# Performance work log

Measured on AMD Instinct MI355X. Metric: run time of the kernel, lower is better.

The kernel has to match this reference:

```python
import jax, jax.numpy as jnp
import numpy as np

N, E = 10000, 100000
WIDTH, KER_WIDTH, DEPTH = 32, 128, 3
EDGE_ATTR_DIM, IN_WIDTH, OUT_WIDTH, COORD_DIM = 6, 3, 1, 3


def _glorot(k, fan_in, fan_out):
    return jax.random.normal(k, (fan_in, fan_out), jnp.float32) / np.sqrt(fan_in).astype(np.float32)


def setup_inputs() -> dict:
    key = jax.random.key(0)
    ks = jax.random.split(key, 16)
    z = lambda n: jnp.zeros((n,), jnp.float32)
    return {
        "x": jax.random.normal(ks[0], (N, IN_WIDTH), jnp.float32),
        "edge_index": jax.random.randint(ks[1], (2, E), 0, N),
        "edge_attr": jax.random.normal(ks[2], (E, EDGE_ATTR_DIM), jnp.float32),
        "coords_init": jax.random.normal(ks[3], (N, COORD_DIM), jnp.float32),
        "fc1_w": _glorot(ks[4], IN_WIDTH, WIDTH), "fc1_b": z(WIDTH),
        "ker_w1": _glorot(ks[5], EDGE_ATTR_DIM + 1, KER_WIDTH // 2), "ker_b1": z(KER_WIDTH // 2),
        "ker_w2": _glorot(ks[6], KER_WIDTH // 2, KER_WIDTH), "ker_b2": z(KER_WIDTH),
        "ker_w3": _glorot(ks[7], KER_WIDTH, WIDTH * WIDTH), "ker_b3": z(WIDTH * WIDTH),
        "cm_w1": _glorot(ks[8], WIDTH, WIDTH), "cm_b1": z(WIDTH),
        "cm_w2": _glorot(ks[9], WIDTH, 1) * 1e-3,  # xavier gain=0.001 coord head, no bias
        "fc2_w1": _glorot(ks[10], WIDTH, 2 * WIDTH), "fc2_b1": z(2 * WIDTH),
        "fc2_w2": _glorot(ks[11], 2 * WIDTH, OUT_WIDTH), "fc2_b2": z(OUT_WIDTH),
    }


def _seg_mean(data, seg, n):
    s = jax.ops.segment_sum(data, seg, num_segments=n)
    c = jax.ops.segment_sum(jnp.ones((seg.shape[0], 1), data.dtype), seg, num_segments=n)
    return s / jnp.clip(c, 1.0)


def reference(x, edge_index, edge_attr, coords_init,
              fc1_w, fc1_b, ker_w1, ker_b1, ker_w2, ker_b2, ker_w3, ker_b3,
              cm_w1, cm_b1, cm_w2, fc2_w1, fc2_b1, fc2_w2, fc2_b2):
    row, col = edge_index[0], edge_index[1]
    h = x @ fc1_w + fc1_b                                   # [N, W]
    coord = coords_init
    for _ in range(DEPTH):
        coord_diff = coord[row] - coord[col]                # [E, 3]
        radial = jnp.sum(coord_diff * coord_diff, axis=-1, keepdims=True)
        kin = jnp.concatenate([edge_attr, radial], axis=-1)  # [E, ker_in]
        k = jax.nn.relu(kin @ ker_w1 + ker_b1)
        k = jax.nn.relu(k @ ker_w2 + ker_b2)
        Wk = (k @ ker_w3 + ker_b3).reshape(E, WIDTH, WIDTH)  # per-edge kernel matrix
        m = jnp.einsum('eij,ej->ei', Wk, h[col])             # per-edge message [E, W]
        phi = jax.nn.relu(m @ cm_w1 + cm_b1) @ cm_w2         # [E, 1]
        coord = coord + _seg_mean(coord_diff * phi, row, N)  # equivariant coord update
        h = jax.nn.relu(h + _seg_mean(m, row, N))            # GKN node update
    out = jax.nn.relu(h @ fc2_w1 + fc2_b1) @ fc2_w2 + fc2_b2  # [N, out_width]
    return out, coord
```

## Files before the change

kernel.cpp:

```cpp
#include <hip/hip_runtime.h>
#include <hip/hip_bf16.h>

#define NN 10000
#define NE 100000
#define NSEG_MAX 16384

typedef __bf16 bf16x8 __attribute__((ext_vector_type(8)));
typedef float  f32x4  __attribute__((ext_vector_type(4)));

__device__ __forceinline__ f32x4 relu4(f32x4 a) {
    a.x = fmaxf(a.x, 0.f); a.y = fmaxf(a.y, 0.f);
    a.z = fmaxf(a.z, 0.f); a.w = fmaxf(a.w, 0.f);
    return a;
}

__device__ __forceinline__ unsigned pk2(float a, float b) {
    unsigned ua = (unsigned)__builtin_bit_cast(unsigned short, (__bf16)a);
    unsigned ub = (unsigned)__builtin_bit_cast(unsigned short, (__bf16)b);
    return ua | (ub << 16);
}

__global__ void k_setup(const float* __restrict__ w3, __bf16* __restrict__ w3t_sw,
                        const float* __restrict__ b3, __bf16* __restrict__ b3t_sw,
                        const float* __restrict__ w2, __bf16* __restrict__ w2t_sw,
                        const float* __restrict__ cw1, __bf16* __restrict__ cmw1_sw,
                        const float* __restrict__ x, const float* __restrict__ fc1w,
                        const float* __restrict__ fc1b, const float* __restrict__ cinit,
                        float* __restrict__ h, float* __restrict__ coord,
                        const int* __restrict__ eidx,
                        int* __restrict__ deg, int* __restrict__ within,
                        int* __restrict__ degc, int* __restrict__ withinc) {
    int t = blockIdx.x * blockDim.x + threadIdx.x;
    if (t < 131072) {
        int jj = t & 7, l = (t >> 3) & 63, ut = t >> 9;
        int u  = ut*16 + (l & 15);
        int j2 = ((l >> 4) & 3)*8 + jj;
        int f  = u >> 9, ll = (u >> 3) & 63, j0 = u & 7;
        int c  = (f & 3)*32 + ((ll >> 4) & 3)*8 + j0;
        int i  = (f >> 2)*16 + (ll & 15);
        w3t_sw[t] = (__bf16)w3[c*1024 + i*32 + j2];
    } else if (t < 132096) {
        int idx = t - 131072;
        int jj = idx & 7, l = (idx >> 3) & 63, tt = idx >> 9;
        int i  = tt*16 + (l & 15);
        int j2 = ((l >> 4) & 3)*8 + jj;
        b3t_sw[idx] = (__bf16)b3[i*32 + j2];
    } else if (t < 140288) {
        int idx = t - 132096;
        int jj = idx & 7, l = (idx >> 3) & 63, g = idx >> 9;
        int ct = g >> 1, ks = g & 1;
        int c  = ct*16 + (l & 15);
        int ch = ks*32 + ((l >> 4) & 3)*8 + jj;
        w2t_sw[idx] = (__bf16)w2[ch*128 + c];
    } else if (t < 142336) {
        int idx = t - 140288;
        int jj = idx & 7, l = (idx >> 3) & 63, ot = idx >> 9;
        int o  = ot*16 + (l & 15);
        int i  = ((l >> 4) & 3)*8 + jj;
        cmw1_sw[idx] = (__bf16)cw1[i*32 + o];
    } else if (t < 142336 + NN) {
        int n = t - 142336;
        float x0 = x[n*3+0], x1 = x[n*3+1], x2 = x[n*3+2];
        #pragma unroll
        for (int j = 0; j < 32; j += 4) {
            f32x4 a = *(const f32x4*)(fc1b + j);
            a += x0 * (*(const f32x4*)(fc1w + 0*32 + j));
            a += x1 * (*(const f32x4*)(fc1w + 1*32 + j));
            a += x2 * (*(const f32x4*)(fc1w + 2*32 + j));
            *(f32x4*)(h + n*32 + j) = a;
        }
        coord[n*3+0] = cinit[n*3+0];
        coord[n*3+1] = cinit[n*3+1];
        coord[n*3+2] = cinit[n*3+2];
    } else if (t < 142336 + NN + NE) {
        int e = t - 142336 - NN;
        within[e] = atomicAdd(&deg[eidx[e]], 1);
    } else if (t < 142336 + NN + 2*NE) {
        int e = t - 142336 - NN - NE;
        withinc[e] = atomicAdd(&degc[eidx[NE + e]], 1);
    }
}

__global__ __launch_bounds__(1024, 1)
void k_scan(const int* __restrict__ deg, int* __restrict__ rowptr,
            float* __restrict__ deg_inv,
            const int* __restrict__ degc, int* __restrict__ colptr,
            int* __restrict__ seg_meta, int* __restrict__ seg_start) {
    __shared__ int ssum[1024];
    const int tid = threadIdx.x;
    const int CH = 10;
    const int base = tid * CH;

    int s = 0;
    for (int i = 0; i < CH; ++i) { int n = base + i; if (n < NN) s += deg[n]; }
    ssum[tid] = s;
    __syncthreads();
    for (int off = 1; off < 1024; off <<= 1) {
        int t = (tid >= off) ? ssum[tid - off] : 0;
        __syncthreads(); ssum[tid] += t; __syncthreads();
    }
    int run = ssum[tid] - s;
    for (int i = 0; i < CH; ++i) {
        int n = base + i;
        if (n < NN) {
            int d = deg[n];
            rowptr[n] = run; run += d;
            deg_inv[n] = 1.0f / (float)(d > 1 ? d : 1);
        }
    }
    if (tid == 1023) rowptr[NN] = ssum[1023];
    __syncthreads();

    s = 0;
    for (int i = 0; i < CH; ++i) { int n = base + i; if (n < NN) s += degc[n]; }
    ssum[tid] = s;
    __syncthreads();
    for (int off = 1; off < 1024; off <<= 1) {
        int t = (tid >= off) ? ssum[tid - off] : 0;
        __syncthreads(); ssum[tid] += t; __syncthreads();
    }
    run = ssum[tid] - s;
    for (int i = 0; i < CH; ++i) {
        int n = base + i;
        if (n < NN) { colptr[n] = run; run += degc[n]; }
    }
    if (tid == 1023) colptr[NN] = ssum[1023];
    __syncthreads();

    s = 0;
    for (int i = 0; i < CH; ++i) { int n = base + i; if (n < NN) s += (degc[n] + 15) >> 4; }
    ssum[tid] = s;
    __syncthreads();
    for (int off = 1; off < 1024; off <<= 1) {
        int t = (tid >= off) ? ssum[tid - off] : 0;
        __syncthreads(); ssum[tid] += t; __syncthreads();
    }
    run = ssum[tid] - s;
    for (int i = 0; i < CH; ++i) {
        int n = base + i;
        if (n < NN) {
            int d = degc[n], ns = (d + 15) >> 4, cp = colptr[n];
            for (int k = 0; k < ns; ++k) {
                int cnt = d - k*16; if (cnt > 16) cnt = 16;
                seg_meta[run + k]  = n | (cnt << 16);
                seg_start[run + k] = cp + k*16;
            }
            run += ns;
        }
    }
    __syncthreads();
    int nseg = ssum[1023];
    for (int sg = nseg + tid; sg < NSEG_MAX; sg += 1024) {
        seg_meta[sg] = -1;
        seg_start[sg] = 0;
    }
}

__global__ void k_setup2(const int* __restrict__ eidx, const float* __restrict__ eattr,
                         const int* __restrict__ rowptr, const int* __restrict__ within,
                         const int* __restrict__ colptr, const int* __restrict__ withinc,
                         int* __restrict__ cs_pos, int* __restrict__ cs_row,
                         float* __restrict__ eattr_cs) {
    int e = blockIdx.x * blockDim.x + threadIdx.x;
    if (e >= NE) return;
    int row = eidx[e], col = eidx[NE + e];
    int pos = rowptr[row] + within[e];
    int cs  = colptr[col] + withinc[e];
    cs_pos[cs] = pos; cs_row[cs] = row;
    #pragma unroll
    for (int a = 0; a < 6; ++a) eattr_cs[(size_t)cs*8 + a] = eattr[(size_t)e*6 + a];
    eattr_cs[(size_t)cs*8 + 6] = 0.f; eattr_cs[(size_t)cs*8 + 7] = 0.f;
}

__global__ __launch_bounds__(512, 4)
void k_edge(const int* __restrict__ seg_meta, const int* __restrict__ seg_start,
            const int* __restrict__ cs_pos, const int* __restrict__ cs_row,
            const float* __restrict__ eattr_cs, const float* __restrict__ coord,
            const float* __restrict__ w1, const float* __restrict__ b1,
            const __bf16* __restrict__ w2t_sw, const float* __restrict__ b2,
            const __bf16* __restrict__ w3t_sw, const __bf16* __restrict__ b3t_sw,
            const float* __restrict__ h,
            const __bf16* __restrict__ cmw1_sw, const float* __restrict__ cm_b1,
            const float* __restrict__ cm_w2,
            float* __restrict__ cds, float* __restrict__ m_s,
            float* __restrict__ phis) {
    __shared__ __bf16 r_lds[8 * 4096];
    const int lane = threadIdx.x & 63;
    const int wave = threadIdx.x >> 6;
    const int q  = lane >> 4;
    const int el = lane & 15;
    const int sb = blockIdx.x * 8;
    if (seg_meta[sb] < 0) return;

    const int m8 = seg_meta[sb + (lane & 7)];
    const int v8 = (m8 < 0) ? 0 : (m8 & 0xFFFF);
    const int vv = __shfl(v8, el & 7, 64);
    const int mown  = __shfl(m8, wave, 64);
    const int cnt   = mown >> 16;
    int start = seg_start[sb + wave];
    start = start < 0 ? 0 : (start > NE - 1 ? NE - 1 : start);

    bf16x8 bfrag = {};
    if (el < 8) {
        const float* hp = h + (size_t)vv * 32 + q * 8;
        f32x4 h0 = *(const f32x4*)hp;
        f32x4 h1 = *(const f32x4*)(hp + 4);
        bfrag[0]=(__bf16)h0.x; bfrag[1]=(__bf16)h0.y; bfrag[2]=(__bf16)h0.z; bfrag[3]=(__bf16)h0.w;
        bfrag[4]=(__bf16)h1.x; bfrag[5]=(__bf16)h1.y; bfrag[6]=(__bf16)h1.z; bfrag[7]=(__bf16)h1.w;
    }

    int slot = start + el; if (slot >= NE) slot = NE - 1;
    const int pos   = cs_pos[slot];
    const int rnode = cs_row[slot];
    const int vn    = __shfl(v8, wave, 64);
    const float dx = coord[rnode*3+0] - coord[vn*3+0];
    const float dy = coord[rnode*3+1] - coord[vn*3+1];
    const float dz = coord[rnode*3+2] - coord[vn*3+2];
    const float rad = dx*dx + dy*dy + dz*dz;
    f32x4 ea0 = *(const f32x4*)(eattr_cs + (size_t)slot*8);
    f32x4 ea1 = *(const f32x4*)(eattr_cs + (size_t)slot*8 + 4);
    const float kin[7] = {ea0.x, ea0.y, ea0.z, ea0.w, ea1.x, ea1.y, rad};

    const f32x4 zero = {0.f, 0.f, 0.f, 0.f};

    #pragma unroll 8
    for (int g = 0; g < 32; ++g) {
        const int ut = wave*32 + g;
        bf16x8 af = *(const bf16x8*)(w3t_sw + ((size_t)ut*64 + lane)*8);
        f32x4 c = __builtin_amdgcn_mfma_f32_16x16x32_bf16(af, bfrag, zero, 0, 0, 0);
        if (el < 8) {
            unsigned u0 = pk2(c.x, c.y);
            unsigned u1 = pk2(c.z, c.w);
            const int lb = el*8192 + ((ut*32 + q*8) ^ (el << 4));
            uint2* dst = (uint2*)((char*)r_lds + lb);
            *dst = make_uint2(u0, u1);
        }
    }

    f32x4 bt0, bt1;
    {
        bf16x8 a0 = *(const bf16x8*)(b3t_sw + ((size_t)0*64 + lane)*8);
        bf16x8 a1 = *(const bf16x8*)(b3t_sw + ((size_t)1*64 + lane)*8);
        bt0 = __builtin_amdgcn_mfma_f32_16x16x32_bf16(a0, bfrag, zero, 0, 0, 0);
        bt1 = __builtin_amdgcn_mfma_f32_16x16x32_bf16(a1, bfrag, zero, 0, 0, 0);
    }
    f32x4 btv0, btv1;
    #pragma unroll
    for (int r = 0; r < 4; ++r) {
        btv0[r] = __shfl(bt0[r], (lane & 48) + wave, 64);
        btv1[r] = __shfl(bt1[r], (lane & 48) + wave, 64);
    }

    bf16x8 k1f[2];
    #pragma unroll
    for (int ks = 0; ks < 2; ++ks) {
        const int c0 = ks*32 + q*8;
        f32x4 a0 = *(const f32x4*)(b1 + c0);
        f32x4 a1 = *(const f32x4*)(b1 + c0 + 4);
        #pragma unroll
        for (int a = 0; a < 7; ++a) {
            const float kv = kin[a];
            a0 += kv * (*(const f32x4*)(w1 + a*64 + c0));
            a1 += kv * (*(const f32x4*)(w1 + a*64 + c0 + 4));
        }
        a0 = relu4(a0); a1 = relu4(a1);
        bf16x8 t;
        t[0]=(__bf16)a0.x; t[1]=(__bf16)a0.y; t[2]=(__bf16)a0.z; t[3]=(__bf16)a0.w;
        t[4]=(__bf16)a1.x; t[5]=(__bf16)a1.y; t[6]=(__bf16)a1.z; t[7]=(__bf16)a1.w;
        k1f[ks] = t;
    }

    f32x4 C2[8];
    #pragma unroll
    for (int ct = 0; ct < 8; ++ct) {
        f32x4 acc = zero;
        #pragma unroll
        for (int ks = 0; ks < 2; ++ks) {
            bf16x8 af = *(const bf16x8*)(w2t_sw + ((ct*2 + ks)*64 + lane)*8);
            acc = __builtin_amdgcn_mfma_f32_16x16x32_bf16(af, k1f[ks], acc, 0, 0, 0);
        }
        f32x4 bb = *(const f32x4*)(b2 + ct*16 + q*4);
        C2[ct] = relu4(acc + bb);
    }

    const int lowq = q & 1, hiq = q >> 1;
    bf16x8 k2f[4];
    #pragma unroll
    for (int ks2 = 0; ks2 < 4; ++ks2) {
        bf16x8 t;
        #pragma unroll
        for (int hh = 0; hh < 2; ++hh) {
            const int src = (lowq*2 + hh)*16 + el;
            #pragma unroll
            for (int rr = 0; rr < 4; ++rr) {
                const float x0 = __shfl(C2[ks2*2][rr],     src, 64);
                const float x1 = __shfl(C2[ks2*2 + 1][rr], src, 64);
                t[hh*4 + rr] = (__bf16)(hiq ? x1 : x0);
            }
        }
        k2f[ks2] = t;
    }

    __syncthreads();
    if (mown < 0) return;

    bf16x8 rA[8];
    #pragma unroll
    for (int f = 0; f < 8; ++f) {
        const int rb = wave*8192 + (((f*64 + lane)*16) ^ (wave << 4));
        rA[f] = *(const bf16x8*)((const char*)r_lds + rb);
    }

    f32x4 M0 = zero, M1 = zero;
    #pragma unroll
    for (int ks2 = 0; ks2 < 4; ++ks2) {
        M0 = __builtin_amdgcn_mfma_f32_16x16x32_bf16(rA[ks2],     k2f[ks2], M0, 0, 0, 0);
        M1 = __builtin_amdgcn_mfma_f32_16x16x32_bf16(rA[4 + ks2], k2f[ks2], M1, 0, 0, 0);
    }
    M0 += btv0; M1 += btv1;

    const bool ev = el < cnt;
    if (ev) {
        *(f32x4*)(m_s + (size_t)pos*32 + q*4)      = M0;
        *(f32x4*)(m_s + (size_t)pos*32 + 16 + q*4) = M1;
        if (q == 0) {
            f32x4 cdv = {dx, dy, dz, rad};
            *(f32x4*)(cds + (size_t)pos*4) = cdv;
        }
    }

    bf16x8 paf;
    #pragma unroll
    for (int hh = 0; hh < 2; ++hh) {
        const int src = (lowq*2 + hh)*16 + el;
        #pragma unroll
        for (int rr = 0; rr < 4; ++rr) {
            const float x0 = __shfl(M0[rr], src, 64);
            const float x1 = __shfl(M1[rr], src, 64);
            paf[hh*4 + rr] = (__bf16)(hiq ? x1 : x0);
        }
    }
    bf16x8 bf0 = *(const bf16x8*)(cmw1_sw + (0*64 + lane)*8);
    bf16x8 bf1 = *(const bf16x8*)(cmw1_sw + (1*64 + lane)*8);
    f32x4 PH0 = __builtin_amdgcn_mfma_f32_16x16x32_bf16(paf, bf0, zero, 0, 0, 0);
    f32x4 PH1 = __builtin_amdgcn_mfma_f32_16x16x32_bf16(paf, bf1, zero, 0, 0, 0);

    const float b1v0 = cm_b1[el], b1v1 = cm_b1[16 + el];
    const float w2v0 = cm_w2[el], w2v1 = cm_w2[16 + el];
    float ph[4]; int pr[4];
    #pragma unroll
    for (int r = 0; r < 4; ++r) {
        float s0 = fmaxf(PH0[r] + b1v0, 0.f) * w2v0
                 + fmaxf(PH1[r] + b1v1, 0.f) * w2v1;
        s0 += __shfl_xor(s0, 1, 64);
        s0 += __shfl_xor(s0, 2, 64);
        s0 += __shfl_xor(s0, 4, 64);
        s0 += __shfl_xor(s0, 8, 64);
        ph[r] = s0;
        pr[r] = __shfl(pos, (q << 4) + q*4 + r, 64);
    }
    if (el == 0) {
        #pragma unroll
        for (int r = 0; r < 4; ++r)
            if (q*4 + r < cnt) phis[pr[r]] = ph[r];
    }
}

__global__ __launch_bounds__(256, 4)
void k_gather(const int* __restrict__ rowptr,
              const float* __restrict__ m_s, const float* __restrict__ phis,
              const float* __restrict__ cds, const float* __restrict__ deg_inv,
              float* __restrict__ coord, float* __restrict__ h,
              const float* __restrict__ fw1, const float* __restrict__ fb1,
              const float* __restrict__ fw2, const float* __restrict__ fb2,
              float* __restrict__ out, int dofinal) {
    int tid = blockIdx.x * blockDim.x + threadIdx.x;
    int n = tid >> 3, sub = tid & 7;
    if (n >= NN) return;
    int st = rowptr[n], en = rowptr[n+1];
    f32x4 am0 = {0.f, 0.f, 0.f, 0.f}, am1 = {0.f, 0.f, 0.f, 0.f};
    int p = st;
    for (; p + 1 < en; p += 2) {
        am0 += *(const f32x4*)(m_s + (size_t)p*32 + sub*4);
        am1 += *(const f32x4*)(m_s + (size_t)(p+1)*32 + sub*4);
    }
    if (p < en) am0 += *(const f32x4*)(m_s + (size_t)p*32 + sub*4);
    f32x4 am = am0 + am1;

    float di = deg_inv[n];
    f32x4 hv = *(const f32x4*)(h + (size_t)n*32 + sub*4);
    hv = relu4(hv + am * di);

    float c0 = 0.f, c1 = 0.f, c2 = 0.f;
    if (sub == 0) {
        float cx0 = 0.f, cy0 = 0.f, cz0 = 0.f;
        float cx1 = 0.f, cy1 = 0.f, cz1 = 0.f;
        int pp = st;
        for (; pp + 1 < en; pp += 2) {
            f32x4 cd0 = *(const f32x4*)(cds + (size_t)pp*4);
            f32x4 cd1 = *(const f32x4*)(cds + (size_t)(pp+1)*4);
            float p0 = phis[pp], p1 = phis[pp+1];
            cx0 += cd0.x * p0; cy0 += cd0.y * p0; cz0 += cd0.z * p0;
            cx1 += cd1.x * p1; cy1 += cd1.y * p1; cz1 += cd1.z * p1;
        }
        if (pp < en) {
            f32x4 cd0 = *(const f32x4*)(cds + (size_t)pp*4);
            float p0 = phis[pp];
            cx0 += cd0.x * p0; cy0 += cd0.y * p0; cz0 += cd0.z * p0;
        }
        c0 = coord[n*3+0] + (cx0 + cx1) * di;
        c1 = coord[n*3+1] + (cy0 + cy1) * di;
        c2 = coord[n*3+2] + (cz0 + cz1) * di;
    }

    if (!dofinal) {
        *(f32x4*)(h + (size_t)n*32 + sub*4) = hv;
        if (sub == 0) {
            coord[n*3+0] = c0; coord[n*3+1] = c1; coord[n*3+2] = c2;
        }
        return;
    }

    const int gbase = (tid & 63) & 56;
    float hreg[32];
    #pragma unroll
    for (int s2 = 0; s2 < 8; ++s2) {
        hreg[s2*4+0] = __shfl(hv.x, gbase + s2, 64);
        hreg[s2*4+1] = __shfl(hv.y, gbase + s2, 64);
        hreg[s2*4+2] = __shfl(hv.z, gbase + s2, 64);
        hreg[s2*4+3] = __shfl(hv.w, gbase + s2, 64);
    }
    float po = 0.f;
    #pragma unroll
    for (int oo = 0; oo < 8; oo += 4) {
        int o = sub*8 + oo;
        f32x4 a = *(const f32x4*)(fb1 + o);
        #pragma unroll
        for (int i = 0; i < 32; ++i)
            a += hreg[i] * (*(const f32x4*)(fw1 + i*64 + o));
        a = relu4(a);
        f32x4 w2 = *(const f32x4*)(fw2 + o);
        po += a.x*w2.x + a.y*w2.y + a.z*w2.z + a.w*w2.w;
    }
    po += __shfl_xor(po, 1, 64);
    po += __shfl_xor(po, 2, 64);
    po += __shfl_xor(po, 4, 64);
    if (sub == 0) {
        out[n] = po + fb2[0];
        out[NN + n*3 + 0] = c0;
        out[NN + n*3 + 1] = c1;
        out[NN + n*3 + 2] = c2;
    }
}


extern "C" void kernel_launch(void* const* d_in, const int* in_sizes, int n_in,
                              void* d_out, int out_size, void* d_ws, size_t ws_size,
                              hipStream_t stream) {
    const float* x      = (const float*)d_in[0];
    const int*   eidx   = (const int*)  d_in[1];
    const float* eattr  = (const float*)d_in[2];
    const float* cinit  = (const float*)d_in[3];
    const float* fc1w   = (const float*)d_in[4];
    const float* fc1b   = (const float*)d_in[5];
    const float* kw1    = (const float*)d_in[6];
    const float* kb1    = (const float*)d_in[7];
    const float* kw2    = (const float*)d_in[8];
    const float* kb2    = (const float*)d_in[9];
    const float* kw3    = (const float*)d_in[10];
    const float* kb3    = (const float*)d_in[11];
    const float* cmw1   = (const float*)d_in[12];
    const float* cmb1   = (const float*)d_in[13];
    const float* cmw2   = (const float*)d_in[14];
    const float* f2w1   = (const float*)d_in[15];
    const float* f2b1   = (const float*)d_in[16];
    const float* f2w2   = (const float*)d_in[17];
    const float* f2b2   = (const float*)d_in[18];
    float* out = (float*)d_out;

    char* p = (char*)d_ws;
    auto carve = [&](size_t bytes) {
        void* r = (void*)p;
        p += (bytes + 255) & ~(size_t)255;
        return r;
    };
    float*  h        = (float*) carve((size_t)NN * 32 * 4);
    float*  coord    = (float*) carve((size_t)NN * 3 * 4);
    int*    deg      = (int*)   carve((size_t)NN * 4);
    float*  deg_inv  = (float*) carve((size_t)NN * 4);
    int*    rowptr   = (int*)   carve((size_t)(NN + 1) * 4);
    int*    within   = (int*)   carve((size_t)NE * 4);
    int*    degc     = (int*)   carve((size_t)NN * 4);
    int*    colptr   = (int*)   carve((size_t)(NN + 1) * 4);
    int*    withinc  = (int*)   carve((size_t)NE * 4);
    int*    cs_pos   = (int*)   carve((size_t)NE * 4);
    int*    cs_row   = (int*)   carve((size_t)NE * 4);
    float*  eattr_cs = (float*) carve((size_t)NE * 8 * 4);
    int*    seg_meta = (int*)   carve((size_t)NSEG_MAX * 4);
    int*    seg_start= (int*)   carve((size_t)NSEG_MAX * 4);
    float*  cds      = (float*) carve((size_t)NE * 4 * 4);
    float*  m_s      = (float*) carve((size_t)NE * 32 * 4);
    float*  phis     = (float*) carve((size_t)NE * 4);
    __bf16* w3t_sw   = (__bf16*)carve((size_t)131072 * 2);
    __bf16* b3t_sw   = (__bf16*)carve((size_t)1024 * 2);
    __bf16* w2t_sw   = (__bf16*)carve((size_t)8192 * 2);
    __bf16* cmw1_sw  = (__bf16*)carve((size_t)2048 * 2);

    const int TB = 256;
    dim3 b(TB);
    const int totS = 142336 + NN + 2*NE;
    dim3 gS((totS + TB - 1) / TB);
    dim3 gS2((NE + TB - 1) / TB);
    dim3 gE(NSEG_MAX / 8);
    dim3 gA((NN*8 + TB - 1) / TB);

    hipMemsetAsync(deg, 0, (size_t)NN * 4, stream);
    hipMemsetAsync(degc, 0, (size_t)NN * 4, stream);
    k_setup<<<gS, b, 0, stream>>>(kw3, w3t_sw, kb3, b3t_sw, kw2, w2t_sw, cmw1, cmw1_sw,
                                  x, fc1w, fc1b, cinit, h, coord, eidx,
                                  deg, within, degc, withinc);
    k_scan<<<1, dim3(1024), 0, stream>>>(deg, rowptr, deg_inv, degc, colptr,
                                         seg_meta, seg_start);
    k_setup2<<<gS2, b, 0, stream>>>(eidx, eattr, rowptr, within, colptr, withinc,
                                    cs_pos, cs_row, eattr_cs);

    for (int d = 0; d < 3; ++d) {
        k_edge<<<gE, dim3(512), 0, stream>>>(seg_meta, seg_start, cs_pos, cs_row,
                                             eattr_cs, coord, kw1, kb1, w2t_sw, kb2,
                                             w3t_sw, b3t_sw, h, cmw1_sw, cmb1, cmw2,
                                             cds, m_s, phis);
        k_gather<<<gA, b, 0, stream>>>(rowptr, m_s, phis, cds, deg_inv, coord, h,
                                       f2w1, f2b1, f2w2, f2b2, out, d == 2 ? 1 : 0);
    }
}
```

Measured before the change: 362.3 us.

## Process 16 segments per 1024-thread block with two-phase W3 projection and LDS weights

The edge kernel now handles 16 column segments per block with 16 waves instead of 8. The W3·h projection into LDS is split into two half-phases separated by barriers so the per-segment buffer halves in size. The w2 and cm_w1 fragments are staged once per block in LDS rather than read from global memory by every wave. Each W3 fragment now projects 16 node vectors per MFMA instead of 8, halving W3 reads per node. The cost is extra barriers and a larger block, which may limit occupancy.

After: 328.4 us. -9.4%, faster.

```diff
diff --git a/kernel.cpp b/kernel.cpp
--- a/kernel.cpp
+++ b/kernel.cpp
@@ -172,7 +172,7 @@
     eattr_cs[(size_t)cs*8 + 6] = 0.f; eattr_cs[(size_t)cs*8 + 7] = 0.f;
 }
 
-__global__ __launch_bounds__(512, 4)
+__global__ __launch_bounds__(1024, 4)
 void k_edge(const int* __restrict__ seg_meta, const int* __restrict__ seg_start,
             const int* __restrict__ cs_pos, const int* __restrict__ cs_row,
             const float* __restrict__ eattr_cs, const float* __restrict__ coord,
@@ -184,25 +184,32 @@
             const float* __restrict__ cm_w2,
             float* __restrict__ cds, float* __restrict__ m_s,
             float* __restrict__ phis) {
-    __shared__ __bf16 r_lds[8 * 4096];
-    const int lane = threadIdx.x & 63;
-    const int wave = threadIdx.x >> 6;
+    __shared__ __align__(16) __bf16 r_lds[16 * 2048];
+    __shared__ __align__(16) __bf16 wlds[10240];
+    const int tid  = threadIdx.x;
+    const int lane = tid & 63;
+    const int wave = tid >> 6;
     const int q  = lane >> 4;
     const int el = lane & 15;
-    const int sb = blockIdx.x * 8;
+    const int sb = blockIdx.x * 16;
     if (seg_meta[sb] < 0) return;
 
-    const int m8 = seg_meta[sb + (lane & 7)];
-    const int v8 = (m8 < 0) ? 0 : (m8 & 0xFFFF);
-    const int vv = __shfl(v8, el & 7, 64);
-    const int mown  = __shfl(m8, wave, 64);
+    {
+        ((f32x4*)wlds)[tid] = ((const f32x4*)w2t_sw)[tid];
+        if (tid < 256) ((f32x4*)(wlds + 8192))[tid] = ((const f32x4*)cmw1_sw)[tid];
+    }
+
+    const int mown = seg_meta[sb + wave];
+    const bool live = mown >= 0;
+    const int v_own = live ? (mown & 0xFFFF) : 0;
     const int cnt   = mown >> 16;
     int start = seg_start[sb + wave];
-    start = start < 0 ? 0 : (start > NE - 1 ? NE - 1 : start);
-
-    bf16x8 bfrag = {};
-    if (el < 8) {
-        const float* hp = h + (size_t)vv * 32 + q * 8;
+
+    const int mel = seg_meta[sb + el];
+    const int vel = (mel < 0) ? 0 : (mel & 0xFFFF);
+    bf16x8 bfrag;
+    {
+        const float* hp = h + (size_t)vel * 32 + q * 8;
         f32x4 h0 = *(const f32x4*)hp;
         f32x4 h1 = *(const f32x4*)(hp + 4);
         bfrag[0]=(__bf16)h0.x; bfrag[1]=(__bf16)h0.y; bfrag[2]=(__bf16)h0.z; bfrag[3]=(__bf16)h0.w;
@@ -212,10 +219,9 @@
     int slot = start + el; if (slot >= NE) slot = NE - 1;
     const int pos   = cs_pos[slot];
     const int rnode = cs_row[slot];
-    const int vn    = __shfl(v8, wave, 64);
-    const float dx = coord[rnode*3+0] - coord[vn*3+0];
-    const float dy = coord[rnode*3+1] - coord[vn*3+1];
-    const float dz = coord[rnode*3+2] - coord[vn*3+2];
+    const float dx = coord[rnode*3+0] - coord[v_own*3+0];
+    const float dy = coord[rnode*3+1] - coord[v_own*3+1];
+    const float dz = coord[rnode*3+2] - coord[v_own*3+2];
     const float rad = dx*dx + dy*dy + dz*dz;
     f32x4 ea0 = *(const f32x4*)(eattr_cs + (size_t)slot*8);
     f32x4 ea1 = *(const f32x4*)(eattr_cs + (size_t)slot*8 + 4);
@@ -223,33 +229,21 @@
 
     const f32x4 zero = {0.f, 0.f, 0.f, 0.f};
 
-    #pragma unroll 8
-    for (int g = 0; g < 32; ++g) {
-        const int ut = wave*32 + g;
-        bf16x8 af = *(const bf16x8*)(w3t_sw + ((size_t)ut*64 + lane)*8);
-        f32x4 c = __builtin_amdgcn_mfma_f32_16x16x32_bf16(af, bfrag, zero, 0, 0, 0);
-        if (el < 8) {
-            unsigned u0 = pk2(c.x, c.y);
-            unsigned u1 = pk2(c.z, c.w);
-            const int lb = el*8192 + ((ut*32 + q*8) ^ (el << 4));
-            uint2* dst = (uint2*)((char*)r_lds + lb);
-            *dst = make_uint2(u0, u1);
-        }
-    }
-
-    f32x4 bt0, bt1;
-    {
-        bf16x8 a0 = *(const bf16x8*)(b3t_sw + ((size_t)0*64 + lane)*8);
-        bf16x8 a1 = *(const bf16x8*)(b3t_sw + ((size_t)1*64 + lane)*8);
-        bt0 = __builtin_amdgcn_mfma_f32_16x16x32_bf16(a0, bfrag, zero, 0, 0, 0);
-        bt1 = __builtin_amdgcn_mfma_f32_16x16x32_bf16(a1, bfrag, zero, 0, 0, 0);
-    }
-    f32x4 btv0, btv1;
-    #pragma unroll
-    for (int r = 0; r < 4; ++r) {
-        btv0[r] = __shfl(bt0[r], (lane & 48) + wave, 64);
-        btv1[r] = __shfl(bt1[r], (lane & 48) + wave, 64);
-    }
+    auto phaseA = [&](int halfsel) {
+        #pragma unroll
+        for (int s = 0; s < 8; ++s) {
+            const int idx = wave*8 + s;
+            const int fh = idx >> 5, g = idx & 31;
+            const int f  = ((fh & 1) | ((fh & 2) << 1)) + halfsel*2;
+            const int ut = f*32 + g;
+            bf16x8 af = *(const bf16x8*)(w3t_sw + ((size_t)ut*64 + lane)*8);
+            f32x4 c = __builtin_amdgcn_mfma_f32_16x16x32_bf16(af, bfrag, zero, 0, 0, 0);
+            const int wb = el*4096 + ((fh*1024 + g*32 + q*8) ^ ((el & 7) << 4));
+            *(uint2*)((char*)r_lds + wb) = make_uint2(pk2(c.x, c.y), pk2(c.z, c.w));
+        }
+    };
+
+    phaseA(0);
 
     bf16x8 k1f[2];
     #pragma unroll
@@ -270,13 +264,15 @@
         k1f[ks] = t;
     }
 
+    __syncthreads();
+
     f32x4 C2[8];
     #pragma unroll
     for (int ct = 0; ct < 8; ++ct) {
         f32x4 acc = zero;
         #pragma unroll
         for (int ks = 0; ks < 2; ++ks) {
-            bf16x8 af = *(const bf16x8*)(w2t_sw + ((ct*2 + ks)*64 + lane)*8);
+            bf16x8 af = *(const bf16x8*)(wlds + ((ct*2 + ks)*64 + lane)*8);
             acc = __builtin_amdgcn_mfma_f32_16x16x32_bf16(af, k1f[ks], acc, 0, 0, 0);
         }
         f32x4 bb = *(const f32x4*)(b2 + ct*16 + q*4);
@@ -301,25 +297,41 @@
         k2f[ks2] = t;
     }
 
-    __syncthreads();
-    if (mown < 0) return;
-
-    bf16x8 rA[8];
-    #pragma unroll
-    for (int f = 0; f < 8; ++f) {
-        const int rb = wave*8192 + (((f*64 + lane)*16) ^ (wave << 4));
-        rA[f] = *(const bf16x8*)((const char*)r_lds + rb);
-    }
-
     f32x4 M0 = zero, M1 = zero;
-    #pragma unroll
-    for (int ks2 = 0; ks2 < 4; ++ks2) {
-        M0 = __builtin_amdgcn_mfma_f32_16x16x32_bf16(rA[ks2],     k2f[ks2], M0, 0, 0, 0);
-        M1 = __builtin_amdgcn_mfma_f32_16x16x32_bf16(rA[4 + ks2], k2f[ks2], M1, 0, 0, 0);
-    }
-    M0 += btv0; M1 += btv1;
-
-    const bool ev = el < cnt;
+    auto mhalf = [&](int k2lo) {
+        bf16x8 rA[4];
+        #pragma unroll
+        for (int fh = 0; fh < 4; ++fh) {
+            const int rb = wave*4096 + ((fh*1024 + lane*16) ^ ((wave & 7) << 4));
+            rA[fh] = *(const bf16x8*)((const char*)r_lds + rb);
+        }
+        M0 = __builtin_amdgcn_mfma_f32_16x16x32_bf16(rA[0], k2f[k2lo],   M0, 0, 0, 0);
+        M0 = __builtin_amdgcn_mfma_f32_16x16x32_bf16(rA[1], k2f[k2lo+1], M0, 0, 0, 0);
+        M1 = __builtin_amdgcn_mfma_f32_16x16x32_bf16(rA[2], k2f[k2lo],   M1, 0, 0, 0);
+        M1 = __builtin_amdgcn_mfma_f32_16x16x32_bf16(rA[3], k2f[k2lo+1], M1, 0, 0, 0);
+    };
+
+    mhalf(0);
+    __syncthreads();
+    phaseA(1);
+    __syncthreads();
+    mhalf(2);
+
+    {
+        bf16x8 a0 = *(const bf16x8*)(b3t_sw + ((size_t)0*64 + lane)*8);
+        bf16x8 a1 = *(const bf16x8*)(b3t_sw + ((size_t)1*64 + lane)*8);
+        f32x4 bt0 = __builtin_amdgcn_mfma_f32_16x16x32_bf16(a0, bfrag, zero, 0, 0, 0);
+        f32x4 bt1 = __builtin_amdgcn_mfma_f32_16x16x32_bf16(a1, bfrag, zero, 0, 0, 0);
+        f32x4 btv0, btv1;
+        #pragma unroll
+        for (int r = 0; r < 4; ++r) {
+            btv0[r] = __shfl(bt0[r], (lane & 48) + wave, 64);
+            btv1[r] = __shfl(bt1[r], (lane & 48) + wave, 64);
+        }
+        M0 += btv0; M1 += btv1;
+    }
+
+    const bool ev = live && (el < cnt);
     if (ev) {
         *(f32x4*)(m_s + (size_t)pos*32 + q*4)      = M0;
         *(f32x4*)(m_s + (size_t)pos*32 + 16 + q*4) = M1;
@@ -340,8 +352,8 @@
             paf[hh*4 + rr] = (__bf16)(hiq ? x1 : x0);
         }
     }
-    bf16x8 bf0 = *(const bf16x8*)(cmw1_sw + (0*64 + lane)*8);
-    bf16x8 bf1 = *(const bf16x8*)(cmw1_sw + (1*64 + lane)*8);
+    bf16x8 bf0 = *(const bf16x8*)(wlds + 8192 + (0*64 + lane)*8);
+    bf16x8 bf1 = *(const bf16x8*)(wlds + 8192 + (1*64 + lane)*8);
     f32x4 PH0 = __builtin_amdgcn_mfma_f32_16x16x32_bf16(paf, bf0, zero, 0, 0, 0);
     f32x4 PH1 = __builtin_amdgcn_mfma_f32_16x16x32_bf16(paf, bf1, zero, 0, 0, 0);
 
@@ -359,7 +371,7 @@
         ph[r] = s0;
         pr[r] = __shfl(pos, (q << 4) + q*4 + r, 64);
     }
-    if (el == 0) {
+    if (live && el == 0) {
         #pragma unroll
         for (int r = 0; r < 4; ++r)
             if (q*4 + r < cnt) phis[pr[r]] = ph[r];
@@ -511,7 +523,7 @@
     const int totS = 142336 + NN + 2*NE;
     dim3 gS((totS + TB - 1) / TB);
     dim3 gS2((NE + TB - 1) / TB);
-    dim3 gE(NSEG_MAX / 8);
+    dim3 gE(NSEG_MAX / 16);
     dim3 gA((NN*8 + TB - 1) / TB);
 
     hipMemsetAsync(deg, 0, (size_t)NN * 4, stream);
@@ -525,10 +537,10 @@
                                     cs_pos, cs_row, eattr_cs);
 
     for (int d = 0; d < 3; ++d) {
-        k_edge<<<gE, dim3(512), 0, stream>>>(seg_meta, seg_start, cs_pos, cs_row,
-                                             eattr_cs, coord, kw1, kb1, w2t_sw, kb2,
-                                             w3t_sw, b3t_sw, h, cmw1_sw, cmb1, cmw2,
-                                             cds, m_s, phis);
+        k_edge<<<gE, dim3(1024), 0, stream>>>(seg_meta, seg_start, cs_pos, cs_row,
+                                              eattr_cs, coord, kw1, kb1, w2t_sw, kb2,
+                                              w3t_sw, b3t_sw, h, cmw1_sw, cmb1, cmw2,
+                                              cds, m_s, phis);
         k_gather<<<gA, b, 0, stream>>>(rowptr, m_s, phis, cds, deg_inv, coord, h,
                                        f2w1, f2b1, f2w2, f2b2, out, d == 2 ? 1 : 0);
     }
```
